# Optimization experiments

Hardware: AMD Instinct MI355X
Metric: run time of the kernel (lower is better)

The kernel has to match this reference:

```python
import jax, jax.numpy as jnp
import numpy as np

B, H, N, D = 4, 8, 2048, 64  # d_model=512, n_heads=8 -> d_head=64
MASK_PROB = 0.1
SCALE = D ** -0.5


def setup_inputs() -> dict:
    key = jax.random.key(0)
    kq, kk, kv, km = jax.random.split(key, 4)
    q = jax.random.normal(kq, (B, H, N, D), dtype=jnp.float32)
    k = jax.random.normal(kk, (B, H, N, D), dtype=jnp.float32)
    v = jax.random.normal(kv, (B, H, N, D), dtype=jnp.float32)
    # torch.bernoulli(full(..., prob)): 1 with prob=mask_prob -> dropped
    mask = jax.random.bernoulli(km, MASK_PROB, (B, H, N, N))
    return {"q": q, "k": k, "v": v, "mask": mask}


def reference(q, k, v, mask):
    # [B,H,N,N] scores: QK^T * scale -> tanh -> zero where mask is True
    scores = jnp.tanh(jnp.einsum("bhnd,bhmd->bhnm", q, k) * SCALE)
    scores = scores * (~mask).astype(scores.dtype)
    return jnp.einsum("bhnm,bhmd->bhnd", scores, v)
```

## Files before the change

### kernel.cpp

```cpp
#include <hip/hip_runtime.h>

namespace {

constexpr int N = 2048;
constexpr int D = 64;
constexpr float SCALE = 0.125f;
constexpr int LK = 72;
constexpr int LV = 68;
constexpr int NT = N / 64;
constexpr size_t NKV = (size_t)4 * 8 * 2048 * 64;

typedef __attribute__((ext_vector_type(8))) short bf16x8;
typedef __attribute__((ext_vector_type(4))) short short4v;
typedef __attribute__((ext_vector_type(2))) short short2v;
typedef __attribute__((ext_vector_type(4))) float f32x4;
typedef __attribute__((ext_vector_type(4))) int   int4v;

__device__ inline short f2bf(float x) {
  union { float f; unsigned u; } a; a.f = x;
  unsigned r = a.u + 0x7fffu + ((a.u >> 16) & 1u);
  return (short)(r >> 16);
}

#if __has_builtin(__builtin_amdgcn_cvt_pk_bf16_f32)
typedef __attribute__((ext_vector_type(2))) __bf16 bfv2;
__device__ inline short2v pk_bf(float lo, float hi) {
  bfv2 t = __builtin_amdgcn_cvt_pk_bf16_f32(lo, hi);
  return __builtin_bit_cast(short2v, t);
}
#else
__device__ inline short2v pk_bf(float lo, float hi) {
  short2v r; r[0] = f2bf(lo); r[1] = f2bf(hi); return r;
}
#endif

__device__ inline short4v pk4(float4 f) {
  short2v a = pk_bf(f.x, f.y), b = pk_bf(f.z, f.w);
  short4v r; r[0] = a[0]; r[1] = a[1]; r[2] = b[0]; r[3] = b[1];
  return r;
}

__device__ inline float fast_tanh(float x) {
  float e = __builtin_amdgcn_exp2f(x * 2.885390081777927f);
  return 1.0f - 2.0f * __builtin_amdgcn_rcpf(e + 1.0f);
}

}

__global__ __launch_bounds__(256) void cvt_kv_bf16(
    const float* __restrict__ K, const float* __restrict__ V,
    short* __restrict__ KB, short* __restrict__ VB)
{
  const int n4 = (int)(NKV / 4);
  const int stride = gridDim.x * blockDim.x;
  for (int j = blockIdx.x * blockDim.x + threadIdx.x; j < n4; j += stride) {
    ((short4v*)KB)[j] = pk4(((const float4*)K)[j]);
    ((short4v*)VB)[j] = pk4(((const float4*)V)[j]);
  }
}

template <bool BF>
__global__ __launch_bounds__(256, 4) void attn_tanh_kernel(
    const float* __restrict__ Q, const void* __restrict__ Kp,
    const void* __restrict__ Vp, const int* __restrict__ M,
    float* __restrict__ O)
{
  __shared__ __align__(16) short k_s[64 * LK];
  __shared__ __align__(16) short s_s[64 * LK];
  __shared__ __align__(16) short vt_s[64 * LV];

  const int tid  = threadIdx.x;
  const int wave = tid >> 6;
  const int lane = tid & 63;
  const int l15  = lane & 15;
  const int quad = lane >> 4;

  const int bh = blockIdx.x & 31;
  const int q0 = (blockIdx.x >> 5) * 64;

  const float* qp = Q + (size_t)bh * N * D;
  const int*   mp = M + (size_t)bh * N * N;
  float* op = O + (size_t)bh * N * D;

  bf16x8 qf[2];
  {
    const float* qrow = qp + (size_t)(q0 + wave * 16 + l15) * D + quad * 8;
#pragma unroll
    for (int ks = 0; ks < 2; ++ks) {
      float4 f0 = *(const float4*)(qrow + ks * 32);
      float4 f1 = *(const float4*)(qrow + ks * 32 + 4);
      short4v lo = pk4(f0), hi = pk4(f1);
      bf16x8 t;
      t[0]=lo[0]; t[1]=lo[1]; t[2]=lo[2]; t[3]=lo[3];
      t[4]=hi[0]; t[5]=hi[1]; t[6]=hi[2]; t[7]=hi[3];
      qf[ks] = t;
    }
  }

  const int*   mbase = mp + (size_t)(q0 + wave * 16 + l15) * N + quad * 4;
  int4v mreg[4];

  const int r0 = tid >> 4;
  const int c4 = (tid & 15) << 2;
  float4 kreg[4];
  float  vregf[16];
  const int krow = tid >> 3;
  const int kcol = (tid & 7) * 8;
  bf16x8 kreg2[2];
  short  vregb[16];

  const float* kpf = nullptr; const float* vpf = nullptr;
  const short* kpb = nullptr; const short* vpb = nullptr;
  const float* vbasef = nullptr; const short* vbaseb = nullptr;
  if constexpr (BF) {
    kpb = (const short*)Kp + (size_t)bh * N * D;
    vpb = (const short*)Vp + (size_t)bh * N * D;
    vbaseb = vpb + (size_t)(wave * 16) * D + lane;
  } else {
    kpf = (const float*)Kp + (size_t)bh * N * D;
    vpf = (const float*)Vp + (size_t)bh * N * D;
    vbasef = vpf + (size_t)(wave * 16) * D + lane;
  }

  auto issue_loads = [&](int kt1) {
    if constexpr (BF) {
      const short* kt_ = kpb + (size_t)kt1 * 64 * D;
#pragma unroll
      for (int i = 0; i < 2; ++i)
        kreg2[i] = *(const bf16x8*)(kt_ + (size_t)(krow + i * 32) * D + kcol);
      const short* vt_ = vbaseb + (size_t)kt1 * 64 * D;
#pragma unroll
      for (int i = 0; i < 16; ++i)
        vregb[i] = vt_[(size_t)i * D];
    } else {
      const float* kt_ = kpf + (size_t)kt1 * 64 * D;
#pragma unroll
      for (int i = 0; i < 4; ++i)
        kreg[i] = *(const float4*)(kt_ + (size_t)(i * 16 + r0) * D + c4);
      const float* vt_ = vbasef + (size_t)kt1 * 64 * D;
#pragma unroll
      for (int i = 0; i < 16; ++i)
        vregf[i] = vt_[(size_t)i * D];
    }
    const int* mb = mbase + (size_t)kt1 * 64;
#pragma unroll
    for (int ct = 0; ct < 4; ++ct)
      mreg[ct] = __builtin_nontemporal_load((const int4v*)(mb + ct * 16));
  };

  auto write_kv = [&]() {
    if constexpr (BF) {
#pragma unroll
      for (int i = 0; i < 2; ++i)
        *(bf16x8*)(&k_s[(krow + i * 32) * LK + kcol]) = kreg2[i];
#pragma unroll
      for (int c = 0; c < 4; ++c) {
        short4v vv;
        vv[0] = vregb[4*c+0]; vv[1] = vregb[4*c+1];
        vv[2] = vregb[4*c+2]; vv[3] = vregb[4*c+3];
        *(short4v*)(&vt_s[lane * LV + wave * 16 + 4 * c]) = vv;
      }
    } else {
#pragma unroll
      for (int i = 0; i < 4; ++i)
        *(short4v*)(&k_s[(i * 16 + r0) * LK + c4]) = pk4(kreg[i]);
#pragma unroll
      for (int c = 0; c < 4; ++c) {
        short2v p0 = pk_bf(vregf[4*c+0], vregf[4*c+1]);
        short2v p1 = pk_bf(vregf[4*c+2], vregf[4*c+3]);
        short4v vv; vv[0]=p0[0]; vv[1]=p0[1]; vv[2]=p1[0]; vv[3]=p1[1];
        *(short4v*)(&vt_s[lane * LV + wave * 16 + 4 * c]) = vv;
      }
    }
  };

  issue_loads(0);

  f32x4 o_acc[4];
#pragma unroll
  for (int i = 0; i < 4; ++i) o_acc[i] = (f32x4){0.f, 0.f, 0.f, 0.f};

  for (int kt = 0; kt < NT; ++kt) {
    __syncthreads();
    write_kv();
    __syncthreads();

    int4v mcur[4];
#pragma unroll
    for (int ct = 0; ct < 4; ++ct) mcur[ct] = mreg[ct];

#pragma unroll
    for (int ct = 0; ct < 4; ++ct) {
      f32x4 acc = {0.f, 0.f, 0.f, 0.f};
#pragma unroll
      for (int ksi = 0; ksi < 2; ++ksi) {
        bf16x8 a = *(const bf16x8*)(&k_s[(ct * 16 + l15) * LK + ksi * 32 + quad * 8]);
        acc = __builtin_amdgcn_mfma_f32_16x16x32_bf16(a, qf[ksi], acc, 0, 0, 0);
      }
      float s0 = mcur[ct][0] ? 0.f : fast_tanh(acc[0] * SCALE);
      float s1 = mcur[ct][1] ? 0.f : fast_tanh(acc[1] * SCALE);
      float s2 = mcur[ct][2] ? 0.f : fast_tanh(acc[2] * SCALE);
      float s3 = mcur[ct][3] ? 0.f : fast_tanh(acc[3] * SCALE);
      short2v p0 = pk_bf(s0, s1), p1 = pk_bf(s2, s3);
      short4v sv; sv[0]=p0[0]; sv[1]=p0[1]; sv[2]=p1[0]; sv[3]=p1[1];
      *(short4v*)(&s_s[(wave * 16 + l15) * LK + ct * 16 + quad * 4]) = sv;
    }

    if (kt + 1 < NT) issue_loads(kt + 1);

#pragma unroll
    for (int ksi = 0; ksi < 2; ++ksi) {
      bf16x8 a = *(const bf16x8*)(&s_s[(wave * 16 + l15) * LK + ksi * 32 + quad * 8]);
#pragma unroll
      for (int nt = 0; nt < 4; ++nt) {
        const short* vb = &vt_s[(nt * 16 + l15) * LV + ksi * 32 + quad * 8];
        short4v lo = *(const short4v*)(vb);
        short4v hi = *(const short4v*)(vb + 4);
        bf16x8 b = __builtin_shufflevector(lo, hi, 0, 1, 2, 3, 4, 5, 6, 7);
        o_acc[nt] = __builtin_amdgcn_mfma_f32_16x16x32_bf16(a, b, o_acc[nt], 0, 0, 0);
      }
    }
  }

#pragma unroll
  for (int nt = 0; nt < 4; ++nt) {
#pragma unroll
    for (int r = 0; r < 4; ++r) {
      op[(q0 + wave * 16 + quad * 4 + r) * D + nt * 16 + l15] = o_acc[nt][r];
    }
  }
}

extern "C" void kernel_launch(void* const* d_in, const int* in_sizes, int n_in,
                              void* d_out, int out_size, void* d_ws, size_t ws_size,
                              hipStream_t stream) {
  const float* q = (const float*)d_in[0];
  const float* k = (const float*)d_in[1];
  const float* v = (const float*)d_in[2];
  const int*   m = (const int*)d_in[3];
  float* out = (float*)d_out;

  if (ws_size >= NKV * 2 * sizeof(short)) {
    short* kb = (short*)d_ws;
    short* vb = kb + NKV;
    cvt_kv_bf16<<<dim3(2048), dim3(256), 0, stream>>>(k, v, kb, vb);
    attn_tanh_kernel<true><<<dim3(1024), dim3(256), 0, stream>>>(q, kb, vb, m, out);
  } else {
    attn_tanh_kernel<false><<<dim3(1024), dim3(256), 0, stream>>>(q, k, v, m, out);
  }
}
```

Measured before the change: 776.5 us.

## Pack int mask into 64-bit bitmasks in a pre-pass kernel

Adds a mask_pack kernel that reads the int32 mask once and uses wave ballots to compress each 64-element row chunk into one 64-bit word. The attention kernel then loads a single u64 per tile instead of four int4 vectors and tests bits. The full mask is read the same number of times (once), so the gain would come only from overlap and load pressure inside the main kernel. The change also drops the fp32 fallback path and assumes the workspace is large enough, which adds an extra launch and a write/read of the packed mask.

```diff
diff --git a/kernel.cpp b/kernel.cpp
--- a/kernel.cpp
+++ b/kernel.cpp
@@ -8,13 +8,15 @@
 constexpr int LK = 72;
 constexpr int LV = 68;
 constexpr int NT = N / 64;
-constexpr size_t NKV = (size_t)4 * 8 * 2048 * 64;
+constexpr int BH = 32;
+constexpr size_t NKV    = (size_t)BH * N * D;
+constexpr size_t NMASK  = (size_t)BH * N * N;
+constexpr size_t NWORDS = NMASK / 64;
 
 typedef __attribute__((ext_vector_type(8))) short bf16x8;
 typedef __attribute__((ext_vector_type(4))) short short4v;
 typedef __attribute__((ext_vector_type(2))) short short2v;
 typedef __attribute__((ext_vector_type(4))) float f32x4;
-typedef __attribute__((ext_vector_type(4))) int   int4v;
 
 __device__ inline short f2bf(float x) {
   union { float f; unsigned u; } a; a.f = x;
@@ -59,10 +61,32 @@
   }
 }
 
-template <bool BF>
+__global__ __launch_bounds__(256) void mask_pack(
+    const int* __restrict__ M, unsigned long long* __restrict__ W)
+{
+  const int lane = threadIdx.x & 63;
+  const size_t g = (size_t)blockIdx.x * 4 + (threadIdx.x >> 6);
+  const size_t steps = NWORDS / 8192;
+  const int* p = M + (g * steps) * 64 + lane;
+  unsigned long long* w = W + g * steps;
+  for (size_t s = 0; s < steps; s += 8) {
+    int v[8];
+#pragma unroll
+    for (int j = 0; j < 8; ++j)
+      v[j] = __builtin_nontemporal_load(p + (s + j) * 64);
+    unsigned long long b[8];
+#pragma unroll
+    for (int j = 0; j < 8; ++j) b[j] = __ballot(v[j] != 0);
+    if (lane == 0) {
+#pragma unroll
+      for (int j = 0; j < 8; ++j) w[s + j] = b[j];
+    }
+  }
+}
+
 __global__ __launch_bounds__(256, 4) void attn_tanh_kernel(
-    const float* __restrict__ Q, const void* __restrict__ Kp,
-    const void* __restrict__ Vp, const int* __restrict__ M,
+    const float* __restrict__ Q, const short* __restrict__ KB,
+    const short* __restrict__ VB, const unsigned long long* __restrict__ MW,
     float* __restrict__ O)
 {
   __shared__ __align__(16) short k_s[64 * LK];
@@ -79,8 +103,12 @@
   const int q0 = (blockIdx.x >> 5) * 64;
 
   const float* qp = Q + (size_t)bh * N * D;
-  const int*   mp = M + (size_t)bh * N * N;
   float* op = O + (size_t)bh * N * D;
+  const short* kpb = KB + (size_t)bh * N * D;
+  const short* vpb = VB + (size_t)bh * N * D;
+  const short* vbase = vpb + (size_t)(wave * 16) * D + lane;
+  const unsigned long long* mwb =
+      MW + ((size_t)bh * N + q0 + wave * 16 + l15) * NT;
 
   bf16x8 qf[2];
   {
@@ -97,80 +125,34 @@
     }
   }
 
-  const int*   mbase = mp + (size_t)(q0 + wave * 16 + l15) * N + quad * 4;
-  int4v mreg[4];
-
-  const int r0 = tid >> 4;
-  const int c4 = (tid & 15) << 2;
-  float4 kreg[4];
-  float  vregf[16];
   const int krow = tid >> 3;
   const int kcol = (tid & 7) * 8;
   bf16x8 kreg2[2];
   short  vregb[16];
-
-  const float* kpf = nullptr; const float* vpf = nullptr;
-  const short* kpb = nullptr; const short* vpb = nullptr;
-  const float* vbasef = nullptr; const short* vbaseb = nullptr;
-  if constexpr (BF) {
-    kpb = (const short*)Kp + (size_t)bh * N * D;
-    vpb = (const short*)Vp + (size_t)bh * N * D;
-    vbaseb = vpb + (size_t)(wave * 16) * D + lane;
-  } else {
-    kpf = (const float*)Kp + (size_t)bh * N * D;
-    vpf = (const float*)Vp + (size_t)bh * N * D;
-    vbasef = vpf + (size_t)(wave * 16) * D + lane;
-  }
+  unsigned long long mreg;
 
   auto issue_loads = [&](int kt1) {
-    if constexpr (BF) {
-      const short* kt_ = kpb + (size_t)kt1 * 64 * D;
-#pragma unroll
-      for (int i = 0; i < 2; ++i)
-        kreg2[i] = *(const bf16x8*)(kt_ + (size_t)(krow + i * 32) * D + kcol);
-      const short* vt_ = vbaseb + (size_t)kt1 * 64 * D;
-#pragma unroll
-      for (int i = 0; i < 16; ++i)
-        vregb[i] = vt_[(size_t)i * D];
-    } else {
-      const float* kt_ = kpf + (size_t)kt1 * 64 * D;
-#pragma unroll
-      for (int i = 0; i < 4; ++i)
-        kreg[i] = *(const float4*)(kt_ + (size_t)(i * 16 + r0) * D + c4);
-      const float* vt_ = vbasef + (size_t)kt1 * 64 * D;
-#pragma unroll
-      for (int i = 0; i < 16; ++i)
-        vregf[i] = vt_[(size_t)i * D];
-    }
-    const int* mb = mbase + (size_t)kt1 * 64;
-#pragma unroll
-    for (int ct = 0; ct < 4; ++ct)
-      mreg[ct] = __builtin_nontemporal_load((const int4v*)(mb + ct * 16));
+    const short* kt_ = kpb + (size_t)kt1 * 64 * D;
+#pragma unroll
+    for (int i = 0; i < 2; ++i)
+      kreg2[i] = *(const bf16x8*)(kt_ + (size_t)(krow + i * 32) * D + kcol);
+    const short* vt_ = vbase + (size_t)kt1 * 64 * D;
+#pragma unroll
+    for (int i = 0; i < 16; ++i)
+      vregb[i] = vt_[(size_t)i * D];
+    mreg = mwb[kt1];
   };
 
   auto write_kv = [&]() {
-    if constexpr (BF) {
-#pragma unroll
-      for (int i = 0; i < 2; ++i)
-        *(bf16x8*)(&k_s[(krow + i * 32) * LK + kcol]) = kreg2[i];
-#pragma unroll
-      for (int c = 0; c < 4; ++c) {
-        short4v vv;
-        vv[0] = vregb[4*c+0]; vv[1] = vregb[4*c+1];
-        vv[2] = vregb[4*c+2]; vv[3] = vregb[4*c+3];
-        *(short4v*)(&vt_s[lane * LV + wave * 16 + 4 * c]) = vv;
-      }
-    } else {
-#pragma unroll
-      for (int i = 0; i < 4; ++i)
-        *(short4v*)(&k_s[(i * 16 + r0) * LK + c4]) = pk4(kreg[i]);
-#pragma unroll
-      for (int c = 0; c < 4; ++c) {
-        short2v p0 = pk_bf(vregf[4*c+0], vregf[4*c+1]);
-        short2v p1 = pk_bf(vregf[4*c+2], vregf[4*c+3]);
-        short4v vv; vv[0]=p0[0]; vv[1]=p0[1]; vv[2]=p1[0]; vv[3]=p1[1];
-        *(short4v*)(&vt_s[lane * LV + wave * 16 + 4 * c]) = vv;
-      }
+#pragma unroll
+    for (int i = 0; i < 2; ++i)
+      *(bf16x8*)(&k_s[(krow + i * 32) * LK + kcol]) = kreg2[i];
+#pragma unroll
+    for (int c = 0; c < 4; ++c) {
+      short4v vv;
+      vv[0] = vregb[4*c+0]; vv[1] = vregb[4*c+1];
+      vv[2] = vregb[4*c+2]; vv[3] = vregb[4*c+3];
+      *(short4v*)(&vt_s[lane * LV + wave * 16 + 4 * c]) = vv;
     }
   };
 
@@ -185,9 +167,7 @@
     write_kv();
     __syncthreads();
 
-    int4v mcur[4];
-#pragma unroll
-    for (int ct = 0; ct < 4; ++ct) mcur[ct] = mreg[ct];
+    const unsigned long long mcur = mreg;
 
 #pragma unroll
     for (int ct = 0; ct < 4; ++ct) {
@@ -197,10 +177,11 @@
         bf16x8 a = *(const bf16x8*)(&k_s[(ct * 16 + l15) * LK + ksi * 32 + quad * 8]);
         acc = __builtin_amdgcn_mfma_f32_16x16x32_bf16(a, qf[ksi], acc, 0, 0, 0);
       }
-      float s0 = mcur[ct][0] ? 0.f : fast_tanh(acc[0] * SCALE);
-      float s1 = mcur[ct][1] ? 0.f : fast_tanh(acc[1] * SCALE);
-      float s2 = mcur[ct][2] ? 0.f : fast_tanh(acc[2] * SCALE);
-      float s3 = mcur[ct][3] ? 0.f : fast_tanh(acc[3] * SCALE);
+      const unsigned mn = (unsigned)(mcur >> (ct * 16 + quad * 4)) & 0xFu;
+      float s0 = (mn & 1u) ? 0.f : fast_tanh(acc[0] * SCALE);
+      float s1 = (mn & 2u) ? 0.f : fast_tanh(acc[1] * SCALE);
+      float s2 = (mn & 4u) ? 0.f : fast_tanh(acc[2] * SCALE);
+      float s3 = (mn & 8u) ? 0.f : fast_tanh(acc[3] * SCALE);
       short2v p0 = pk_bf(s0, s1), p1 = pk_bf(s2, s3);
       short4v sv; sv[0]=p0[0]; sv[1]=p0[1]; sv[2]=p1[0]; sv[3]=p1[1];
       *(short4v*)(&s_s[(wave * 16 + l15) * LK + ct * 16 + quad * 4]) = sv;
@@ -240,12 +221,11 @@
   const int*   m = (const int*)d_in[3];
   float* out = (float*)d_out;
 
-  if (ws_size >= NKV * 2 * sizeof(short)) {
-    short* kb = (short*)d_ws;
-    short* vb = kb + NKV;
-    cvt_kv_bf16<<<dim3(2048), dim3(256), 0, stream>>>(k, v, kb, vb);
-    attn_tanh_kernel<true><<<dim3(1024), dim3(256), 0, stream>>>(q, kb, vb, m, out);
-  } else {
-    attn_tanh_kernel<false><<<dim3(1024), dim3(256), 0, stream>>>(q, k, v, m, out);
-  }
-}
+  short* kb = (short*)d_ws;
+  short* vb = kb + NKV;
+  unsigned long long* mw = (unsigned long long*)(vb + NKV);
+
+  cvt_kv_bf16<<<dim3(2048), dim3(256), 0, stream>>>(k, v, kb, vb);
+  mask_pack<<<dim3(2048), dim3(256), 0, stream>>>(m, mw);
+  attn_tanh_kernel<<<dim3(1024), dim3(256), 0, stream>>>(q, kb, vb, mw, out);
+}
```

Measured after the change: 787.6 us. Within noise of the previous version (+1.4%).
